# Optimization experiments

Measured on AMD Instinct MI355X. Metric: run time of the kernel, lower is better.

## Reference

```python
import jax, jax.numpy as jnp
import numpy as np

DIM = 512
HEADS = 8
WIN = 64
HIDDEN = 2048
EPS = 1e-5


def layernorm(x, g, b):
    mu = jnp.mean(x, axis=-1, keepdims=True)
    var = jnp.var(x, axis=-1, keepdims=True)
    return (x - mu) * jax.lax.rsqrt(var + EPS) * g + b


def setup_inputs() -> dict:
    key = jax.random.key(0)
    ks = jax.random.split(key, 10)
    s = lambda fan_in: 1.0 / np.sqrt(fan_in)
    return {
        "x": jax.random.normal(ks[0], (8, 4096, DIM), dtype=jnp.float32),
        "ln1_g": jnp.ones((DIM,), jnp.float32),
        "ln1_b": jnp.zeros((DIM,), jnp.float32),
        "qkv_w": jax.random.normal(ks[1], (DIM, 3 * DIM), jnp.float32) * s(DIM),
        "qkv_b": jnp.zeros((3 * DIM,), jnp.float32),
        "proj_w": jax.random.normal(ks[2], (DIM, DIM), jnp.float32) * s(DIM),
        "proj_b": jnp.zeros((DIM,), jnp.float32),
        "ln2_g": jnp.ones((DIM,), jnp.float32),
        "ln2_b": jnp.zeros((DIM,), jnp.float32),
        "fc1_w": jax.random.normal(ks[3], (DIM, HIDDEN), jnp.float32) * s(DIM),
        "fc1_b": jnp.zeros((HIDDEN,), jnp.float32),
        "fc2_w": jax.random.normal(ks[4], (HIDDEN, DIM), jnp.float32) * s(HIDDEN),
        "fc2_b": jnp.zeros((DIM,), jnp.float32),
    }


def reference(x, ln1_g, ln1_b, qkv_w, qkv_b, proj_w, proj_b, ln2_g, ln2_b,
              fc1_w, fc1_b, fc2_w, fc2_b):
    B, N, C = x.shape
    hd = C // HEADS
    scale = hd ** -0.5

    # --- W-MSA (shift_size forced to 0, attn_mask None) ---
    h = layernorm(x, ln1_g, ln1_b)
    hw = h.reshape(B * (N // WIN), WIN, C)
    qkv = hw @ qkv_w + qkv_b
    qkv = qkv.reshape(-1, WIN, 3, HEADS, hd)
    q = qkv[:, :, 0] * scale
    k = qkv[:, :, 1]
    v = qkv[:, :, 2]
    attn = jnp.einsum('bqhd,bkhd->bhqk', q, k)
    attn = jax.nn.softmax(attn, axis=-1)
    o = jnp.einsum('bhqk,bkhd->bqhd', attn, v).reshape(-1, WIN, C)
    o = o @ proj_w + proj_b
    x = x + o.reshape(B, N, C)

    # --- MLP (GELU exact, dropout=0) ---
    h2 = layernorm(x, ln2_g, ln2_b)
    h2 = jax.nn.gelu(h2 @ fc1_w + fc1_b, approximate=False)
    x = x + (h2 @ fc2_w + fc2_b)
    return x
```

## Files before the change

kernel.cpp:

```cpp
#include <hip/hip_runtime.h>
#include <hip/hip_bf16.h>
#include <cstdint>

typedef unsigned short U16;
typedef float f32x4 __attribute__((ext_vector_type(4)));
typedef __bf16 bf16x8 __attribute__((ext_vector_type(8)));

#define DEVINL __device__ __forceinline__

DEVINL U16 f2bf(float f) {
    unsigned u = __float_as_uint(f);
    return (U16)((u + 0x7FFFu + ((u >> 16) & 1u)) >> 16);
}
DEVINL float bf2f(U16 s) { return __uint_as_float(((unsigned)s) << 16); }

DEVINL void gld16(const void* g, void* l) {
    __builtin_amdgcn_global_load_lds(
        (const __attribute__((address_space(1))) void*)g,
        (__attribute__((address_space(3))) void*)l, 16, 0, 0);
}

#define MFMA_BF16 __builtin_amdgcn_mfma_f32_16x16x32_bf16

__global__ __launch_bounds__(256) void tcast_kernel(const float* __restrict__ w,
                                                    U16* __restrict__ wt, int K, int N) {
    __shared__ float tile[32][33];
    int n0 = blockIdx.x * 32, k0 = blockIdx.y * 32;
    int tx = threadIdx.x, ty = threadIdx.y;
#pragma unroll
    for (int i = 0; i < 32; i += 8) tile[ty + i][tx] = w[(size_t)(k0 + ty + i) * N + (n0 + tx)];
    __syncthreads();
#pragma unroll
    for (int i = 0; i < 32; i += 8) wt[(size_t)(n0 + ty + i) * K + (k0 + tx)] = f2bf(tile[tx][ty + i]);
}

__global__ __launch_bounds__(256) void ln_kernel(const float* __restrict__ x,
                                                 const float* __restrict__ g,
                                                 const float* __restrict__ b,
                                                 U16* __restrict__ out) {
    int lane = threadIdx.x & 63;
    size_t row = (size_t)blockIdx.x * 4 + (threadIdx.x >> 6);
    const float4* xr = (const float4*)(x + row * 512);
    float4 v0 = xr[lane], v1 = xr[lane + 64];
    float s = (v0.x + v0.y) + (v0.z + v0.w) + (v1.x + v1.y) + (v1.z + v1.w);
    float sq = (v0.x * v0.x + v0.y * v0.y + v0.z * v0.z + v0.w * v0.w) +
               (v1.x * v1.x + v1.y * v1.y + v1.z * v1.z + v1.w * v1.w);
#pragma unroll
    for (int m = 1; m < 64; m <<= 1) { s += __shfl_xor(s, m); sq += __shfl_xor(sq, m); }
    float mu = s * (1.f / 512.f);
    float var = sq * (1.f / 512.f) - mu * mu;
    float rs = rsqrtf(var + 1e-5f);
    const float4* g4 = (const float4*)g;
    const float4* b4 = (const float4*)b;
    float4 gv = g4[lane], bv = b4[lane];
    ushort4 o;
    o.x = f2bf((v0.x - mu) * rs * gv.x + bv.x);
    o.y = f2bf((v0.y - mu) * rs * gv.y + bv.y);
    o.z = f2bf((v0.z - mu) * rs * gv.z + bv.z);
    o.w = f2bf((v0.w - mu) * rs * gv.w + bv.w);
    ((ushort4*)(out + row * 512))[lane] = o;
    gv = g4[lane + 64]; bv = b4[lane + 64];
    o.x = f2bf((v1.x - mu) * rs * gv.x + bv.x);
    o.y = f2bf((v1.y - mu) * rs * gv.y + bv.y);
    o.z = f2bf((v1.z - mu) * rs * gv.z + bv.z);
    o.w = f2bf((v1.w - mu) * rs * gv.w + bv.w);
    ((ushort4*)(out + row * 512))[lane + 64] = o;
}

template <int EPI, int K>
__global__ __launch_bounds__(512, 1) void gemm_rt(const U16* __restrict__ A,
                                                  const U16* __restrict__ Bt,
                                                  const float* __restrict__ bias,
                                                  const float* __restrict__ resid,
                                                  U16* __restrict__ outb,
                                                  float* __restrict__ outf,
                                                  int M, int N, int gridN) {
    __shared__ __align__(16) U16 smem[65536];

    const int tid = threadIdx.x;
    const int lane = tid & 63, wv = tid >> 6;
    const int lo = lane & 15, hi = lane >> 4;
    const int wm = wv >> 2, wn = wv & 3;

    const int nwg = gridDim.x, bid = blockIdx.x;
    const int swzb = (bid & 7) * (nwg >> 3) + (bid >> 3);
    const int bn = swzb % gridN, bm = swzb / gridN;

    const int sr2 = tid >> 3;
    const int lc8 = (tid & 7) ^ (sr2 & 7);
    const U16* gAh = A + (size_t)(bm * 256 + sr2) * K + lc8 * 8;
    const U16* gBh = Bt + (size_t)(bn * 256 + sr2) * K + lc8 * 8;

#define SA0(t)                                                              \
    do { U16* _l = smem + ((t) & 1) * 32768 + tid * 8;                      \
         gld16(gAh + (t) * 64, _l);                                         \
         gld16(gAh + (size_t)64 * K + (t) * 64, _l + 4096); } while (0)
#define SA1(t)                                                              \
    do { U16* _l = smem + ((t) & 1) * 32768 + 8192 + tid * 8;               \
         gld16(gAh + (size_t)128 * K + (t) * 64, _l);                       \
         gld16(gAh + (size_t)192 * K + (t) * 64, _l + 4096); } while (0)
#define SB0(t)                                                              \
    do { U16* _l = smem + ((t) & 1) * 32768 + 16384 + tid * 8;              \
         gld16(gBh + (t) * 64, _l);                                         \
         gld16(gBh + (size_t)64 * K + (t) * 64, _l + 4096); } while (0)
#define SB1(t)                                                              \
    do { U16* _l = smem + ((t) & 1) * 32768 + 24576 + tid * 8;              \
         gld16(gBh + (size_t)128 * K + (t) * 64, _l);                       \
         gld16(gBh + (size_t)192 * K + (t) * 64, _l + 4096); } while (0)

    const int ck0 = (hi ^ (lo & 7)) << 3;
    const int ck1 = ((4 | hi) ^ (lo & 7)) << 3;
    const int abase = wm * 8192 + lo * 64;
    const int bbase = 16384 + (wn >> 1) * 8192 + ((wn & 1) * 64 + lo) * 64;

    f32x4 acc[8][4] = {};

    constexpr int NT = K >> 6;
    static_assert(NT >= 4 && (NT % 4) == 0, "K must be a multiple of 256");

    SA0(0); SA1(0); SB0(0); SB1(0);
    SB0(1); SB1(1);
    asm volatile("s_waitcnt vmcnt(4)" ::: "memory");
    __builtin_amdgcn_s_barrier();

#define ITER(s)                                                                 \
    do {                                                                        \
        const int _cb = ((s) & 1) * 32768;                                      \
        const U16* _Ab = smem + _cb + abase;                                    \
        const U16* _Bb = smem + _cb + bbase;                                    \
        bf16x8 af[4][2], bg[4][2], af2[4][2];                                   \
              \
        _Pragma("unroll") for (int i = 0; i < 4; ++i) {                         \
            af[i][0] = *(const bf16x8*)(_Ab + i * 1024 + ck0);                  \
            af[i][1] = *(const bf16x8*)(_Ab + i * 1024 + ck1);                  \
        }                                                                       \
        _Pragma("unroll") for (int j = 0; j < 2; ++j) {                         \
            bg[j][0] = *(const bf16x8*)(_Bb + j * 1024 + ck0);                  \
            bg[j][1] = *(const bf16x8*)(_Bb + j * 1024 + ck1);                  \
        }                                                                       \
        if ((s) + 1 < NT) SA0((s) + 1);                                         \
        __builtin_amdgcn_s_barrier();                                           \
        __builtin_amdgcn_s_setprio(1);                                          \
        _Pragma("unroll") for (int i = 0; i < 4; ++i)                           \
            _Pragma("unroll") for (int j = 0; j < 2; ++j) {                     \
                acc[i][j] = MFMA_BF16(af[i][0], bg[j][0], acc[i][j], 0, 0, 0);  \
                acc[i][j] = MFMA_BF16(af[i][1], bg[j][1], acc[i][j], 0, 0, 0);  \
            }                                                                   \
        __builtin_amdgcn_s_setprio(0);                                          \
        __builtin_amdgcn_s_barrier();                                           \
                    \
        _Pragma("unroll") for (int j = 2; j < 4; ++j) {                         \
            bg[j][0] = *(const bf16x8*)(_Bb + j * 1024 + ck0);                  \
            bg[j][1] = *(const bf16x8*)(_Bb + j * 1024 + ck1);                  \
        }                                                                       \
        if ((s) + 1 < NT) SA1((s) + 1);                                         \
        __builtin_amdgcn_s_barrier();                                           \
        __builtin_amdgcn_s_setprio(1);                                          \
        _Pragma("unroll") for (int i = 0; i < 4; ++i)                           \
            _Pragma("unroll") for (int j = 2; j < 4; ++j) {                     \
                acc[i][j] = MFMA_BF16(af[i][0], bg[j][0], acc[i][j], 0, 0, 0);  \
                acc[i][j] = MFMA_BF16(af[i][1], bg[j][1], acc[i][j], 0, 0, 0);  \
            }                                                                   \
        __builtin_amdgcn_s_setprio(0);                                          \
        __builtin_amdgcn_s_barrier();                                           \
                     \
        _Pragma("unroll") for (int i = 0; i < 4; ++i) {                         \
            af2[i][0] = *(const bf16x8*)(_Ab + 4096 + i * 1024 + ck0);          \
            af2[i][1] = *(const bf16x8*)(_Ab + 4096 + i * 1024 + ck1);          \
        }                                                                       \
        if ((s) + 2 < NT) SB0((s) + 2);                                         \
        __builtin_amdgcn_s_barrier();                                           \
        __builtin_amdgcn_s_setprio(1);                                          \
        _Pragma("unroll") for (int i = 0; i < 4; ++i)                           \
            _Pragma("unroll") for (int j = 0; j < 2; ++j) {                     \
                acc[4 + i][j] = MFMA_BF16(af2[i][0], bg[j][0], acc[4 + i][j], 0, 0, 0); \
                acc[4 + i][j] = MFMA_BF16(af2[i][1], bg[j][1], acc[4 + i][j], 0, 0, 0); \
            }                                                                   \
        __builtin_amdgcn_s_setprio(0);                                          \
        __builtin_amdgcn_s_barrier();                                           \
                              \
        if ((s) + 2 < NT) SB1((s) + 2);                                         \
        __builtin_amdgcn_s_setprio(1);                                          \
        _Pragma("unroll") for (int i = 0; i < 4; ++i)                           \
            _Pragma("unroll") for (int j = 2; j < 4; ++j) {                     \
                acc[4 + i][j] = MFMA_BF16(af2[i][0], bg[j][0], acc[4 + i][j], 0, 0, 0); \
                acc[4 + i][j] = MFMA_BF16(af2[i][1], bg[j][1], acc[4 + i][j], 0, 0, 0); \
            }                                                                   \
        __builtin_amdgcn_s_setprio(0);                                          \
        if ((s) + 2 < NT) {                                                     \
            asm volatile("s_waitcnt vmcnt(4)" ::: "memory");                    \
        } else {                                                                \
            asm volatile("s_waitcnt vmcnt(0)" ::: "memory");                    \
        }                                                                       \
        __builtin_amdgcn_s_barrier();                                           \
    } while (0)

#pragma unroll
    for (int s = 0; s < NT; ++s) ITER(s);

    const int row0 = bm * 256 + wm * 128 + hi * 4;
    const int col0 = bn * 256 + wn * 64 + lo;
    float bc[4];
#pragma unroll
    for (int j = 0; j < 4; ++j) bc[j] = bias[col0 + j * 16];

    if (EPI == 1) {
#pragma unroll
        for (int i = 0; i < 8; ++i)
#pragma unroll
            for (int r = 0; r < 4; ++r) {
                const size_t rowb = (size_t)(row0 + i * 16 + r) * N;
#pragma unroll
                for (int j = 0; j < 4; ++j) {
                    const size_t idx = rowb + col0 + j * 16;
                    outf[idx] = acc[i][j][r] + bc[j] + resid[idx];
                }
            }
    } else {
#pragma unroll
        for (int i = 0; i < 8; ++i)
#pragma unroll
            for (int j = 0; j < 4; ++j)
#pragma unroll
                for (int r = 0; r < 4; ++r) {
                    float v = acc[i][j][r] + bc[j];
                    if (EPI == 2) {
                        float u = v * (0.7978845608028654f + 0.0356774081f * v * v);
                        v = v / (1.f + __expf(-2.f * u));
                    }
                    outb[(size_t)(row0 + i * 16 + r) * N + col0 + j * 16] = f2bf(v);
                }
    }
#undef ITER
#undef SA0
#undef SA1
#undef SB0
#undef SB1
}

__global__ __launch_bounds__(256) void attn_kernel(const U16* __restrict__ qkv,
                                                   U16* __restrict__ o) {
    const int blk = blockIdx.x;
    const int w = blk >> 3, h = blk & 7;
    const int tid = threadIdx.x;
    const int lane = tid & 63, wv = tid >> 6;
    const int lo = lane & 15, hi = lane >> 4;

    __shared__ __align__(16) U16 Qs[64][72];
    __shared__ __align__(16) U16 Ks[64][72];
    __shared__ __align__(16) U16 Vt[64][72];
    __shared__ __align__(16) U16 Ps[4][16][72];

    {
        const int r = tid >> 2;
        const int c0 = (tid & 3) << 4;
        const U16* p = qkv + (size_t)(w * 64 + r) * 1536 + h * 64 + c0;
        *(bf16x8*)&Ks[r][c0] = *(const bf16x8*)(p + 512);
        *(bf16x8*)&Ks[r][c0 + 8] = *(const bf16x8*)(p + 520);
        const U16* pv = p + 1024;
#pragma unroll
        for (int i = 0; i < 16; i++) Vt[c0 + i][r] = pv[i];
#pragma unroll
        for (int i = 0; i < 16; i++) Qs[r][c0 + i] = f2bf(bf2f(p[i]) * 0.125f);
    }
    __syncthreads();

    const int rb = wv * 16;
    f32x4 s[4] = {};
#pragma unroll
    for (int dc = 0; dc < 64; dc += 32) {
        bf16x8 a = *(const bf16x8*)&Qs[rb + lo][dc + hi * 8];
#pragma unroll
        for (int jb = 0; jb < 4; jb++) {
            bf16x8 bfr = *(const bf16x8*)&Ks[jb * 16 + lo][dc + hi * 8];
            s[jb] = MFMA_BF16(a, bfr, s[jb], 0, 0, 0);
        }
    }
#pragma unroll
    for (int r = 0; r < 4; r++) {
        float m = fmaxf(fmaxf(s[0][r], s[1][r]), fmaxf(s[2][r], s[3][r]));
#pragma unroll
        for (int msk = 1; msk < 16; msk <<= 1) m = fmaxf(m, __shfl_xor(m, msk));
        float e[4], sum = 0.f;
#pragma unroll
        for (int jb = 0; jb < 4; jb++) { e[jb] = __expf(s[jb][r] - m); sum += e[jb]; }
#pragma unroll
        for (int msk = 1; msk < 16; msk <<= 1) sum += __shfl_xor(sum, msk);
        float inv = 1.f / sum;
#pragma unroll
        for (int jb = 0; jb < 4; jb++) Ps[wv][hi * 4 + r][jb * 16 + lo] = f2bf(e[jb] * inv);
    }
    __syncthreads();

    f32x4 oa[4] = {};
#pragma unroll
    for (int jc = 0; jc < 64; jc += 32) {
        bf16x8 a = *(const bf16x8*)&Ps[wv][lo][jc + hi * 8];
#pragma unroll
        for (int db = 0; db < 4; db++) {
            bf16x8 bfr = *(const bf16x8*)&Vt[db * 16 + lo][jc + hi * 8];
            oa[db] = MFMA_BF16(a, bfr, oa[db], 0, 0, 0);
        }
    }
#pragma unroll
    for (int db = 0; db < 4; db++)
#pragma unroll
        for (int r = 0; r < 4; r++)
            o[(size_t)(w * 64 + rb + hi * 4 + r) * 512 + h * 64 + db * 16 + lo] = f2bf(oa[db][r]);
}

extern "C" void kernel_launch(void* const* d_in, const int* in_sizes, int n_in,
                              void* d_out, int out_size, void* d_ws, size_t ws_size,
                              hipStream_t stream) {
    const float* x = (const float*)d_in[0];
    const float* ln1_g = (const float*)d_in[1];
    const float* ln1_b = (const float*)d_in[2];
    const float* qkv_w = (const float*)d_in[3];
    const float* qkv_b = (const float*)d_in[4];
    const float* proj_w = (const float*)d_in[5];
    const float* proj_b = (const float*)d_in[6];
    const float* ln2_g = (const float*)d_in[7];
    const float* ln2_b = (const float*)d_in[8];
    const float* fc1_w = (const float*)d_in[9];
    const float* fc1_b = (const float*)d_in[10];
    const float* fc2_w = (const float*)d_in[11];
    const float* fc2_b = (const float*)d_in[12];
    float* out = (float*)d_out;

    char* ws = (char*)d_ws;
    U16* hbuf = (U16*)ws;
    U16* big = (U16*)(ws + 33554432);
    U16* wt_qkv = (U16*)(ws + 33554432 + 134217728);
    U16* wt_proj = wt_qkv + 1536 * 512;
    U16* wt_fc1 = wt_proj + 512 * 512;
    U16* wt_fc2 = wt_fc1 + 2048 * 512;

    dim3 tb(32, 8);
    tcast_kernel<<<dim3(1536 / 32, 512 / 32), tb, 0, stream>>>(qkv_w, wt_qkv, 512, 1536);
    tcast_kernel<<<dim3(512 / 32, 512 / 32), tb, 0, stream>>>(proj_w, wt_proj, 512, 512);
    tcast_kernel<<<dim3(2048 / 32, 512 / 32), tb, 0, stream>>>(fc1_w, wt_fc1, 512, 2048);
    tcast_kernel<<<dim3(512 / 32, 2048 / 32), tb, 0, stream>>>(fc2_w, wt_fc2, 2048, 512);

    ln_kernel<<<8192, 256, 0, stream>>>(x, ln1_g, ln1_b, hbuf);
    gemm_rt<0, 512><<<768, 512, 0, stream>>>(hbuf, wt_qkv, qkv_b, nullptr, big, nullptr, 32768, 1536, 6);
    attn_kernel<<<4096, 256, 0, stream>>>(big, hbuf);
    gemm_rt<1, 512><<<256, 512, 0, stream>>>(hbuf, wt_proj, proj_b, x, nullptr, out, 32768, 512, 2);
    ln_kernel<<<8192, 256, 0, stream>>>(out, ln2_g, ln2_b, hbuf);
    gemm_rt<2, 512><<<1024, 512, 0, stream>>>(hbuf, wt_fc1, fc1_b, nullptr, big, nullptr, 32768, 2048, 8);
    gemm_rt<1, 2048><<<256, 512, 0, stream>>>(big, wt_fc2, fc2_b, out, nullptr, out, 32768, 512, 2);
}
```

Baseline: 352.5 us.

## Fuse proj GEMM with LayerNorm2 and use 128x128 GEMM for MLP

Adds a projection kernel in which each block owns 128 full 512-column rows. It adds the residual, writes x, computes row statistics through shuffles and LDS, and writes the normalized bf16 activations directly. This removes the separate LN2 kernel and one full read of the fp32 intermediate. It also adds a smaller 128x128-tile GEMM with four blocks per CU for fc1 and fc2, trading per-block reuse for more blocks and better latency hiding. The fused kernel reads and writes the same buffer in place, which is only safe because each block touches only its own rows and finishes all loads before storing.

Measured after the change: 379.2 us. 1.08x slower.

```diff
diff --git a/kernel.cpp b/kernel.cpp
--- a/kernel.cpp
+++ b/kernel.cpp
@@ -68,7 +68,126 @@
 }
 
 template <int EPI, int K>
-__global__ __launch_bounds__(512, 1) void gemm_rt(const U16* __restrict__ A,
+__global__ __launch_bounds__(256, 4) void gemm128(const U16* __restrict__ A,
+                                                  const U16* __restrict__ Bt,
+                                                  const float* __restrict__ bias,
+                                                  const float* __restrict__ resid,
+                                                  U16* __restrict__ outb,
+                                                  float* __restrict__ outf,
+                                                  int M, int N, int gridN) {
+    __shared__ __align__(16) U16 smem[16384];
+
+    const int tid = threadIdx.x;
+    const int lane = tid & 63, wv = tid >> 6;
+    const int lo = lane & 15, hi = lane >> 4;
+    const int wm = wv >> 1, wn = wv & 1;
+
+    const int nwg = gridDim.x, bid = blockIdx.x;
+    const int swzb = (bid & 7) * (nwg >> 3) + (bid >> 3);
+    const int bn = swzb % gridN, bm = swzb / gridN;
+
+    const int sr = tid >> 2;
+    const int lc = (tid & 3) ^ ((sr >> 1) & 3);
+    const U16* gA0 = A + (size_t)(bm * 128 + sr) * K + lc * 8;
+    const U16* gA1 = gA0 + (size_t)64 * K;
+    const U16* gB0 = Bt + (size_t)(bn * 128 + sr) * K + lc * 8;
+    const U16* gB1 = gB0 + (size_t)64 * K;
+
+#define STAGE(t2)                                                     \
+    do {                                                              \
+        U16* _l = smem + ((t2) & 1) * 8192 + tid * 8;                 \
+        gld16(gA0 + (t2) * 32, _l);                                   \
+        gld16(gA1 + (t2) * 32, _l + 2048);                            \
+        gld16(gB0 + (t2) * 32, _l + 4096);                            \
+        gld16(gB1 + (t2) * 32, _l + 6144);                            \
+    } while (0)
+
+    const int ck = (hi ^ ((lo >> 1) & 3)) << 3;
+
+    f32x4 acc[4][4] = {};
+
+    constexpr int NT = K >> 5;
+    static_assert(NT >= 16 && (NT % 16) == 0, "K must be a multiple of 512");
+
+    STAGE(0);
+
+    auto tile = [&](int t, bool pf) __attribute__((always_inline)) {
+        if (pf) {
+            STAGE(t + 1);
+            asm volatile("s_waitcnt vmcnt(4)" ::: "memory");
+        } else {
+            asm volatile("s_waitcnt vmcnt(0)" ::: "memory");
+        }
+        __builtin_amdgcn_s_barrier();
+
+        const int cb = (t & 1) * 8192;
+        const U16* Ab = smem + cb + (wm * 64 + lo) * 32 + ck;
+        const U16* Bb = smem + cb + 4096 + (wn * 64 + lo) * 32 + ck;
+
+        bf16x8 af[4], bg[4];
+#pragma unroll
+        for (int i = 0; i < 4; ++i) af[i] = *(const bf16x8*)(Ab + i * 512);
+#pragma unroll
+        for (int j = 0; j < 4; ++j) bg[j] = *(const bf16x8*)(Bb + j * 512);
+
+        __builtin_amdgcn_s_setprio(1);
+#pragma unroll
+        for (int i = 0; i < 4; ++i)
+#pragma unroll
+            for (int j = 0; j < 4; ++j)
+                acc[i][j] = MFMA_BF16(af[i], bg[j], acc[i][j], 0, 0, 0);
+        __builtin_amdgcn_s_setprio(0);
+        __builtin_amdgcn_s_barrier();
+    };
+
+    for (int t0 = 0; t0 + 16 < NT; t0 += 16) {
+#pragma unroll
+        for (int tt = 0; tt < 16; ++tt) tile(t0 + tt, true);
+    }
+#pragma unroll
+    for (int tt = 0; tt < 16; ++tt) {
+        const int t = NT - 16 + tt;
+        tile(t, t + 1 < NT);
+    }
+
+    const int row0 = bm * 128 + wm * 64 + hi * 4;
+    const int col0 = bn * 128 + wn * 64 + lo;
+    float bc[4];
+#pragma unroll
+    for (int j = 0; j < 4; ++j) bc[j] = bias[col0 + j * 16];
+
+    if (EPI == 1) {
+#pragma unroll
+        for (int i = 0; i < 4; ++i)
+#pragma unroll
+            for (int r = 0; r < 4; ++r) {
+                const size_t rowb = (size_t)(row0 + i * 16 + r) * N;
+#pragma unroll
+                for (int j = 0; j < 4; ++j) {
+                    const size_t idx = rowb + col0 + j * 16;
+                    outf[idx] = acc[i][j][r] + bc[j] + resid[idx];
+                }
+            }
+    } else {
+#pragma unroll
+        for (int i = 0; i < 4; ++i)
+#pragma unroll
+            for (int j = 0; j < 4; ++j)
+#pragma unroll
+                for (int r = 0; r < 4; ++r) {
+                    float v = acc[i][j][r] + bc[j];
+                    if (EPI == 2) {
+                        float u = v * (0.7978845608028654f + 0.0356774081f * v * v);
+                        v = v / (1.f + __expf(-2.f * u));
+                    }
+                    outb[(size_t)(row0 + i * 16 + r) * N + col0 + j * 16] = f2bf(v);
+                }
+    }
+#undef STAGE
+}
+
+template <int EPI, int K>
+__global__ __launch_bounds__(512, 1) void gemm256(const U16* __restrict__ A,
                                                   const U16* __restrict__ Bt,
                                                   const float* __restrict__ bias,
                                                   const float* __restrict__ resid,
@@ -129,7 +248,6 @@
         const U16* _Ab = smem + _cb + abase;                                    \
         const U16* _Bb = smem + _cb + bbase;                                    \
         bf16x8 af[4][2], bg[4][2], af2[4][2];                                   \
-              \
         _Pragma("unroll") for (int i = 0; i < 4; ++i) {                         \
             af[i][0] = *(const bf16x8*)(_Ab + i * 1024 + ck0);                  \
             af[i][1] = *(const bf16x8*)(_Ab + i * 1024 + ck1);                  \
@@ -148,7 +266,6 @@
             }                                                                   \
         __builtin_amdgcn_s_setprio(0);                                          \
         __builtin_amdgcn_s_barrier();                                           \
-                    \
         _Pragma("unroll") for (int j = 2; j < 4; ++j) {                         \
             bg[j][0] = *(const bf16x8*)(_Bb + j * 1024 + ck0);                  \
             bg[j][1] = *(const bf16x8*)(_Bb + j * 1024 + ck1);                  \
@@ -163,7 +280,6 @@
             }                                                                   \
         __builtin_amdgcn_s_setprio(0);                                          \
         __builtin_amdgcn_s_barrier();                                           \
-                     \
         _Pragma("unroll") for (int i = 0; i < 4; ++i) {                         \
             af2[i][0] = *(const bf16x8*)(_Ab + 4096 + i * 1024 + ck0);          \
             af2[i][1] = *(const bf16x8*)(_Ab + 4096 + i * 1024 + ck1);          \
@@ -178,7 +294,6 @@
             }                                                                   \
         __builtin_amdgcn_s_setprio(0);                                          \
         __builtin_amdgcn_s_barrier();                                           \
-                              \
         if ((s) + 2 < NT) SB1((s) + 2);                                         \
         __builtin_amdgcn_s_setprio(1);                                          \
         _Pragma("unroll") for (int i = 0; i < 4; ++i)                           \
@@ -236,6 +351,143 @@
 #undef SA1
 #undef SB0
 #undef SB1
+}
+
+template <int K>
+__global__ __launch_bounds__(512, 1) void projln_kernel(const U16* __restrict__ A,
+                                                        const U16* __restrict__ Bt,
+                                                        const float* __restrict__ bias,
+                                                        const float* __restrict__ x,
+                                                        const float* __restrict__ g2,
+                                                        const float* __restrict__ b2,
+                                                        float* __restrict__ xout,
+                                                        U16* __restrict__ h2out) {
+    __shared__ __align__(16) U16 smem[61440];
+    __shared__ float red[2304];
+
+    const int tid = threadIdx.x;
+    const int lane = tid & 63, wv = tid >> 6;
+    const int lo = lane & 15, hi = lane >> 4;
+
+    const int nwg = gridDim.x, bid = blockIdx.x;
+    const int bm = (bid & 7) * (nwg >> 3) + (bid >> 3);
+
+    const int sr = tid >> 2;
+    const int lc = (tid & 3) ^ ((sr >> 1) & 3);
+    const U16* gA0 = A + (size_t)(bm * 128 + sr) * K + lc * 8;
+    const U16* gB0 = Bt + (size_t)sr * K + lc * 8;
+    const U16* gB1 = gB0 + (size_t)128 * K;
+    const U16* gB2 = gB0 + (size_t)256 * K;
+    const U16* gB3 = gB0 + (size_t)384 * K;
+
+#define PSTAGE(t2)                                                    \
+    do {                                                              \
+        U16* _l = smem + ((t2) % 3) * 20480 + tid * 8;                \
+        gld16(gA0 + (t2) * 32, _l);                                   \
+        gld16(gB0 + (t2) * 32, _l + 4096);                            \
+        gld16(gB1 + (t2) * 32, _l + 8192);                            \
+        gld16(gB2 + (t2) * 32, _l + 12288);                           \
+        gld16(gB3 + (t2) * 32, _l + 16384);                           \
+    } while (0)
+
+    const int ck = (hi ^ ((lo >> 1) & 3)) << 3;
+    const int aoff = lo * 32 + ck;
+    const int boff = 4096 + (wv * 64 + lo) * 32 + ck;
+
+    f32x4 acc[8][4] = {};
+
+    constexpr int NT = K >> 5;
+    static_assert(NT == 16, "projln expects K=512");
+
+    PSTAGE(0);
+    PSTAGE(1);
+
+#define PITER(t)                                                                \
+    do {                                                                        \
+        if ((t) + 1 < NT) {                                                     \
+            asm volatile("s_waitcnt vmcnt(5)" ::: "memory");                    \
+        } else {                                                                \
+            asm volatile("s_waitcnt vmcnt(0)" ::: "memory");                    \
+        }                                                                       \
+        __builtin_amdgcn_s_barrier();                                           \
+        if ((t) + 2 < NT) PSTAGE((t) + 2);                                      \
+        {                                                                       \
+            const int _cb = ((t) % 3) * 20480;                                  \
+            const U16* _Ab = smem + _cb + aoff;                                 \
+            const U16* _Bb = smem + _cb + boff;                                 \
+            bf16x8 af[8], bg[4];                                                \
+            _Pragma("unroll") for (int i = 0; i < 8; ++i)                       \
+                af[i] = *(const bf16x8*)(_Ab + i * 512);                        \
+            _Pragma("unroll") for (int j = 0; j < 4; ++j)                       \
+                bg[j] = *(const bf16x8*)(_Bb + j * 512);                        \
+            __builtin_amdgcn_s_setprio(1);                                      \
+            _Pragma("unroll") for (int i = 0; i < 8; ++i)                       \
+                _Pragma("unroll") for (int j = 0; j < 4; ++j)                   \
+                    acc[i][j] = MFMA_BF16(af[i], bg[j], acc[i][j], 0, 0, 0);    \
+            __builtin_amdgcn_s_setprio(0);                                      \
+        }                                                                       \
+    } while (0)
+
+#pragma unroll
+    for (int t = 0; t < NT; ++t) PITER(t);
+
+    const size_t row0g = (size_t)bm * 128;
+    float bc[4];
+#pragma unroll
+    for (int j = 0; j < 4; ++j) bc[j] = bias[wv * 64 + j * 16 + lo];
+
+#pragma unroll
+    for (int i = 0; i < 8; ++i)
+#pragma unroll
+        for (int r = 0; r < 4; ++r) {
+            const int row = i * 16 + hi * 4 + r;
+            const size_t rowb = (row0g + row) * 512;
+            float s = 0.f, sq = 0.f;
+#pragma unroll
+            for (int j = 0; j < 4; ++j) {
+                const int col = wv * 64 + j * 16 + lo;
+                float v = acc[i][j][r] + bc[j] + x[rowb + col];
+                acc[i][j][r] = v;
+                xout[rowb + col] = v;
+                s += v; sq += v * v;
+            }
+#pragma unroll
+            for (int m = 1; m < 16; m <<= 1) { s += __shfl_xor(s, m); sq += __shfl_xor(sq, m); }
+            if (lo == 0) { red[row * 8 + wv] = s; red[1024 + row * 8 + wv] = sq; }
+        }
+    __syncthreads();
+    if (tid < 128) {
+        float s = 0.f, q = 0.f;
+#pragma unroll
+        for (int w = 0; w < 8; ++w) { s += red[tid * 8 + w]; q += red[1024 + tid * 8 + w]; }
+        float mu = s * (1.f / 512.f);
+        float var = q * (1.f / 512.f) - mu * mu;
+        red[2048 + tid] = mu;
+        red[2176 + tid] = rsqrtf(var + 1e-5f);
+    }
+    __syncthreads();
+    float gv[4], bv[4];
+#pragma unroll
+    for (int j = 0; j < 4; ++j) {
+        const int col = wv * 64 + j * 16 + lo;
+        gv[j] = g2[col]; bv[j] = b2[col];
+    }
+#pragma unroll
+    for (int i = 0; i < 8; ++i)
+#pragma unroll
+        for (int r = 0; r < 4; ++r) {
+            const int row = i * 16 + hi * 4 + r;
+            const float mu = red[2048 + row];
+            const float rs = red[2176 + row];
+            const size_t rowb = (row0g + row) * 512;
+#pragma unroll
+            for (int j = 0; j < 4; ++j) {
+                const int col = wv * 64 + j * 16 + lo;
+                h2out[rowb + col] = f2bf((acc[i][j][r] - mu) * rs * gv[j] + bv[j]);
+            }
+        }
+#undef PITER
+#undef PSTAGE
 }
 
 __global__ __launch_bounds__(256) void attn_kernel(const U16* __restrict__ qkv,
@@ -342,10 +594,9 @@
     tcast_kernel<<<dim3(512 / 32, 2048 / 32), tb, 0, stream>>>(fc2_w, wt_fc2, 2048, 512);
 
     ln_kernel<<<8192, 256, 0, stream>>>(x, ln1_g, ln1_b, hbuf);
-    gemm_rt<0, 512><<<768, 512, 0, stream>>>(hbuf, wt_qkv, qkv_b, nullptr, big, nullptr, 32768, 1536, 6);
+    gemm256<0, 512><<<768, 512, 0, stream>>>(hbuf, wt_qkv, qkv_b, nullptr, big, nullptr, 32768, 1536, 6);
     attn_kernel<<<4096, 256, 0, stream>>>(big, hbuf);
-    gemm_rt<1, 512><<<256, 512, 0, stream>>>(hbuf, wt_proj, proj_b, x, nullptr, out, 32768, 512, 2);
-    ln_kernel<<<8192, 256, 0, stream>>>(out, ln2_g, ln2_b, hbuf);
-    gemm_rt<2, 512><<<1024, 512, 0, stream>>>(hbuf, wt_fc1, fc1_b, nullptr, big, nullptr, 32768, 2048, 8);
-    gemm_rt<1, 2048><<<256, 512, 0, stream>>>(big, wt_fc2, fc2_b, out, nullptr, out, 32768, 512, 2);
-}
+    projln_kernel<512><<<256, 512, 0, stream>>>(hbuf, wt_proj, proj_b, x, ln2_g, ln2_b, out, hbuf);
+    gemm128<2, 512><<<4096, 256, 0, stream>>>(hbuf, wt_fc1, fc1_b, nullptr, big, nullptr, 32768, 2048, 16);
+    gemm128<1, 2048><<<1024, 256, 0, stream>>>(big, wt_fc2, fc2_b, out, nullptr, out, 32768, 512, 4);
+}
```
